# Kernel tuning notes

Measured on AMD Instinct MI355X. Metric: run time of the kernel, lower is better.

Reference implementation:

```python
import jax, jax.numpy as jnp
import numpy as np

_EPSILON = 1e-06


def _allocation(usage):
    """Freeness-based allocation: sort usage, exclusive cumprod, scatter back.

    usage: [B, M] in [0, 1]. Returns allocation weights [B, M].
    """
    usage = _EPSILON + (1.0 - _EPSILON) * usage
    nonusage = 1.0 - usage
    m = usage.shape[-1]
    sorted_nonusage, indices = jax.lax.top_k(nonusage, k=m)  # descending nonusage = ascending usage
    sorted_usage = 1.0 - sorted_nonusage
    # exclusive cumulative product along the sorted memory axis
    prod_sorted_usage = jnp.concatenate(
        [jnp.ones_like(sorted_usage[:, :1]),
         jnp.cumprod(sorted_usage, axis=1)[:, :-1]], axis=1)
    sorted_allocation = sorted_nonusage * prod_sorted_usage
    # invert the permutation and gather back to original slot order
    inverse_indices = jnp.argsort(indices, axis=1)
    return jnp.take_along_axis(sorted_allocation, inverse_indices, axis=1)


def _updated_usage(write_weights, free_gate, read_weights, prev_usage):
    """Freeness.__call__: usage after write then after read/free. [B, M]."""
    ww = jax.lax.stop_gradient(write_weights)
    # usage after write: increase toward 1 at written slots
    write_w = 1.0 - jnp.prod(1.0 - ww, axis=1)          # [B, M]
    usage = prev_usage + (1.0 - prev_usage) * write_w
    # usage after read: decrease where free_gate*read_weights is high
    free_read = free_gate[:, :, None] * read_weights      # [B, R, M]
    phi = jnp.prod(1.0 - free_read, axis=1)               # [B, M]
    return usage * phi


def _write_allocation_weights(usage, write_gates, num_writes):
    """Per-write-head allocation weights. Returns [B, num_writes, M]."""
    wg = write_gates[:, :, None]                          # [B, W, 1]
    allocs = []
    for i in range(num_writes):  # small fixed head count; sequential by construction
        a = _allocation(usage)
        allocs.append(a)
        usage = usage + (1.0 - usage) * wg[:, i, :] * a
    return jnp.stack(allocs, axis=1)


def setup_inputs() -> dict:
    key = jax.random.key(0)
    ks = jax.random.split(key, 5)
    B, W, R, M = 512, 4, 8, 16384
    return {
        "write_weights": jax.random.uniform(ks[0], (B, W, M), dtype=jnp.float32),
        "free_gate": jax.random.uniform(ks[1], (B, R), dtype=jnp.float32),
        "read_weights": jax.random.uniform(ks[2], (B, R, M), dtype=jnp.float32),
        "prev_usage": jax.random.uniform(ks[3], (B, M), dtype=jnp.float32),
        "write_gates": jax.random.uniform(ks[4], (B, W), dtype=jnp.float32),
        "num_writes": W,
    }


def reference(write_weights, free_gate, read_weights, prev_usage, write_gates, num_writes):
    usage = _updated_usage(write_weights, free_gate, read_weights, prev_usage)
    alloc = _write_allocation_weights(usage, write_gates, num_writes)
    return usage, alloc
```

## Files before the change

### kernel.cpp

```cpp
#include <hip/hip_runtime.h>
#include <stdint.h>

typedef unsigned long long u64;
typedef unsigned int u32;

#define NBINS 512
#define CAP 512
#define LOG_CUT (-64.0f)
#define LOG_SCALE 20.0f
#define NT 512

template <int TW, int TR>
__global__ __launch_bounds__(NT, 4)
void fused_kernel(const float* __restrict__ ww,
                  const float* __restrict__ fg,
                  const float* __restrict__ rw,
                  const float* __restrict__ prev,
                  const float* __restrict__ wgt,
                  float* __restrict__ out_usage,
                  float* __restrict__ out_alloc,
                  int B, int W, int R, int M)
{
    __shared__ u64   keyS[CAP];
    __shared__ float logS[CAP];
    __shared__ u32   hC[NBINS];
    __shared__ u32   tc[8];
    __shared__ float tw[8];
    __shared__ int   misc[4];
    extern __shared__ float uS[];

    const int Wl = TW > 0 ? TW : W;
    const int Rl = TR > 0 ? TR : R;
    const int b = blockIdx.x;
    const int t = threadIdx.x;
    const int lane = t & 63;
    const int wid = t >> 6;

    const float C1 = (float)(1.0 - 1e-6);
    const float CE = 1e-6f;

    {
        const size_t rowOff = (size_t)b * M;
        float frs[TR > 0 ? TR : 8];
        if (TR > 0)
            #pragma unroll
            for (int r = 0; r < Rl; ++r) frs[r] = fg[(size_t)b * Rl + r];

        const float4 z = make_float4(0.f, 0.f, 0.f, 0.f);
        for (int m = t * 4; m < M; m += NT * 4) {
            const float4 pv = *(const float4*)(prev + rowOff + m);
            float pr0 = 1.f, pr1 = 1.f, pr2 = 1.f, pr3 = 1.f;
            #pragma unroll
            for (int w = 0; w < Wl; ++w) {
                const float4 a = *(const float4*)(ww + ((size_t)b * Wl + w) * M + m);
                pr0 *= (1.0f - a.x); pr1 *= (1.0f - a.y);
                pr2 *= (1.0f - a.z); pr3 *= (1.0f - a.w);
            }
            float u0 = pv.x + (1.0f - pv.x) * (1.0f - pr0);
            float u1 = pv.y + (1.0f - pv.y) * (1.0f - pr1);
            float u2 = pv.z + (1.0f - pv.z) * (1.0f - pr2);
            float u3 = pv.w + (1.0f - pv.w) * (1.0f - pr3);
            float f0 = 1.f, f1 = 1.f, f2 = 1.f, f3 = 1.f;
            #pragma unroll
            for (int r = 0; r < Rl; ++r) {
                const float fr = (TR > 0) ? frs[r] : fg[(size_t)b * Rl + r];
                const float4 a = *(const float4*)(rw + ((size_t)b * Rl + r) * M + m);
                f0 *= (1.0f - fr * a.x); f1 *= (1.0f - fr * a.y);
                f2 *= (1.0f - fr * a.z); f3 *= (1.0f - fr * a.w);
            }
            float4 uo;
            uo.x = u0 * f0; uo.y = u1 * f1; uo.z = u2 * f2; uo.w = u3 * f3;
            *(float4*)(uS + m) = uo;
            *(float4*)(out_usage + rowOff + m) = uo;
            #pragma unroll
            for (int w = 0; w < Wl; ++w)
                *(float4*)(out_alloc + ((size_t)b * Wl + w) * M + m) = z;
        }
    }

    for (int i = 0; i < Wl; ++i) {
        const float wgi = wgt[(size_t)b * Wl + i];
        float* orow = out_alloc + ((size_t)b * Wl + i) * M;

        hC[t] = 0u;
        if (t == 0) { misc[0] = 0; misc[1] = -1; misc[2] = NBINS; }
        __syncthreads();

        for (int x = t * 4; x < M; x += NT * 4) {
            const float4 uu = *(const float4*)(uS + x);
            const float ua[4] = {uu.x, uu.y, uu.z, uu.w};
            #pragma unroll
            for (int j = 0; j < 4; ++j) {
                const float ue = CE + C1 * ua[j];
                const float lg = __log2f(ue);
                int bkt = (int)(-lg * LOG_SCALE);
                bkt = bkt < 0 ? 0 : (bkt > NBINS - 1 ? NBINS - 1 : bkt);
                atomicAdd(&hC[bkt], 1u);
            }
        }
        __syncthreads();

        {
            const int x = NBINS - 1 - t;
            const u32 c = hC[x];
            u32 sc = c;
            float sw = -(float)x * (1.0f / LOG_SCALE) * (float)c;
            #pragma unroll
            for (int off = 1; off < 64; off <<= 1) {
                const u32  oc = __shfl_up(sc, off);
                const float ow = __shfl_up(sw, off);
                if (lane >= off) { sc += oc; sw += ow; }
            }
            if (lane == 63) { tc[wid] = sc; tw[wid] = sw; }
            __syncthreads();
            u32 ac = 0; float aw = 0.f;
            for (int q = 0; q < wid; ++q) { ac += tc[q]; aw += tw[q]; }
            sc += ac; sw += aw;
            if (sw <= LOG_CUT) atomicMax(&misc[1], x);
            if (sc <= (u32)CAP) atomicMin(&misc[2], x);
        }
        __syncthreads();
        const int xs = misc[1];
        const int xc = misc[2];
        const int cut = (xs > xc) ? xs : xc;

        for (int x = t; x < M; x += NT) {
            const float u = uS[x];
            const float ue = CE + C1 * u;
            const float lg = __log2f(ue);
            int bkt = (int)(-lg * LOG_SCALE);
            bkt = bkt < 0 ? 0 : (bkt > NBINS - 1 ? NBINS - 1 : bkt);
            const bool pred = (bkt >= cut) && (cut < NBINS);
            const u64 mask = __ballot(pred);
            const int cnt = __popcll(mask);
            if (cnt) {
                int base = 0;
                if (lane == 0) base = atomicAdd(&misc[0], cnt);
                base = __shfl(base, 0);
                if (pred) {
                    const int pos = base + __popcll(mask & ((1ull << lane) - 1));
                    if (pos < CAP) {
                        const float nn = 1.0f - ue;
                        keyS[pos] = (((u64)(~__float_as_uint(nn))) << 14) | (u64)(u32)x;
                        logS[pos] = lg;
                    }
                }
            }
        }
        __syncthreads();
        int K = misc[0]; if (K > CAP) K = CAP;

        if (t < K) {
            const u64 mykey = keyS[t];
            float S = 0.0f;
            #pragma unroll 4
            for (int k = 0; k < K; ++k) {
                const u64 kk = keyS[k];
                const float lg = logS[k];
                if (kk < mykey) S += lg;
            }
            const float nn = __uint_as_float(~((u32)(mykey >> 14)));
            const int idx = (int)(mykey & 0x3FFFull);
            const float al = nn * __builtin_exp2f(S);
            if (al != 0.0f) {
                orow[idx] = al;
                const float u0v = uS[idx];
                uS[idx] = u0v + ((1.0f - u0v) * wgi) * al;
            }
        }
        __syncthreads();
    }
}

extern "C" void kernel_launch(void* const* d_in, const int* in_sizes, int n_in,
                              void* d_out, int out_size, void* d_ws, size_t ws_size,
                              hipStream_t stream) {
    const float* ww   = (const float*)d_in[0];
    const float* fg   = (const float*)d_in[1];
    const float* rw   = (const float*)d_in[2];
    const float* prev = (const float*)d_in[3];
    const float* wgt  = (const float*)d_in[4];
    const int BWM = in_sizes[0];
    const int BR  = in_sizes[1];
    const int BM  = in_sizes[3];
    const int BW  = in_sizes[4];
    const int M = BWM / BW;
    const int B = BM / M;
    const int W = BW / B;
    const int R = BR / B;

    float* out_usage = (float*)d_out;
    float* out_alloc = out_usage + (size_t)BM;

    const size_t smem = (size_t)M * sizeof(float);
    if (W == 4 && R == 8) {
        hipLaunchKernelGGL((fused_kernel<4, 8>), dim3(B), dim3(NT), smem, stream,
                           ww, fg, rw, prev, wgt, out_usage, out_alloc, B, W, R, M);
    } else {
        hipLaunchKernelGGL((fused_kernel<0, 0>), dim3(B), dim3(NT), smem, stream,
                           ww, fg, rw, prev, wgt, out_usage, out_alloc, B, W, R, M);
    }
}
```

Measured before the change: 163.2 us.

## Write allocation rows densely from shared bitmap instead of zero-fill plus scatter

Drops the upfront zero-fill of all allocation rows and the scattered global stores of the sparse nonzero entries. A per-row bitmap of selected slots plus a prefix-sum rank places each candidate value in compact shared storage, and a final pass writes each full row with float4 stores. Inputs for the usage phase are now loaded all at once before computing, which allows more loads in flight. In exchange it adds extra shared-memory passes, a shared atomicOr per candidate, and additional synchronisation per write head.

After: 168.5 us. +3.3%, slower.

```diff
diff --git a/kernel.cpp b/kernel.cpp
--- a/kernel.cpp
+++ b/kernel.cpp
@@ -9,6 +9,8 @@
 #define LOG_CUT (-64.0f)
 #define LOG_SCALE 20.0f
 #define NT 512
+#define NWAVE (NT / 64)
+#define MAXW 256
 
 template <int TW, int TR>
 __global__ __launch_bounds__(NT, 4)
@@ -23,9 +25,12 @@
 {
     __shared__ u64   keyS[CAP];
     __shared__ float logS[CAP];
+    __shared__ float valS[CAP];
     __shared__ u32   hC[NBINS];
-    __shared__ u32   tc[8];
-    __shared__ float tw[8];
+    __shared__ u64   bmS[MAXW];
+    __shared__ u32   boS[MAXW];
+    __shared__ u32   tc[NWAVE];
+    __shared__ float twv[NWAVE];
     __shared__ int   misc[4];
     extern __shared__ float uS[];
 
@@ -35,26 +40,35 @@
     const int t = threadIdx.x;
     const int lane = t & 63;
     const int wid = t >> 6;
+    const int MW = M >> 6;
 
     const float C1 = (float)(1.0 - 1e-6);
     const float CE = 1e-6f;
 
     {
         const size_t rowOff = (size_t)b * M;
+        const float* wp0 = ww + (size_t)b * Wl * M;
+        const float* rp0 = rw + (size_t)b * Rl * M;
         float frs[TR > 0 ? TR : 8];
-        if (TR > 0)
-            #pragma unroll
-            for (int r = 0; r < Rl; ++r) frs[r] = fg[(size_t)b * Rl + r];
-
-        const float4 z = make_float4(0.f, 0.f, 0.f, 0.f);
+        #pragma unroll
+        for (int r = 0; r < Rl; ++r) frs[r] = fg[(size_t)b * Rl + r];
+
         for (int m = t * 4; m < M; m += NT * 4) {
             const float4 pv = *(const float4*)(prev + rowOff + m);
+            float4 wv[TW > 0 ? TW : 4];
+            float4 rv[TR > 0 ? TR : 8];
+            #pragma unroll
+            for (int w = 0; w < Wl; ++w)
+                wv[w] = *(const float4*)(wp0 + (size_t)w * M + m);
+            #pragma unroll
+            for (int r = 0; r < Rl; ++r)
+                rv[r] = *(const float4*)(rp0 + (size_t)r * M + m);
+
             float pr0 = 1.f, pr1 = 1.f, pr2 = 1.f, pr3 = 1.f;
             #pragma unroll
             for (int w = 0; w < Wl; ++w) {
-                const float4 a = *(const float4*)(ww + ((size_t)b * Wl + w) * M + m);
-                pr0 *= (1.0f - a.x); pr1 *= (1.0f - a.y);
-                pr2 *= (1.0f - a.z); pr3 *= (1.0f - a.w);
+                pr0 *= (1.0f - wv[w].x); pr1 *= (1.0f - wv[w].y);
+                pr2 *= (1.0f - wv[w].z); pr3 *= (1.0f - wv[w].w);
             }
             float u0 = pv.x + (1.0f - pv.x) * (1.0f - pr0);
             float u1 = pv.y + (1.0f - pv.y) * (1.0f - pr1);
@@ -63,18 +77,14 @@
             float f0 = 1.f, f1 = 1.f, f2 = 1.f, f3 = 1.f;
             #pragma unroll
             for (int r = 0; r < Rl; ++r) {
-                const float fr = (TR > 0) ? frs[r] : fg[(size_t)b * Rl + r];
-                const float4 a = *(const float4*)(rw + ((size_t)b * Rl + r) * M + m);
-                f0 *= (1.0f - fr * a.x); f1 *= (1.0f - fr * a.y);
-                f2 *= (1.0f - fr * a.z); f3 *= (1.0f - fr * a.w);
+                const float fr = frs[r];
+                f0 *= (1.0f - fr * rv[r].x); f1 *= (1.0f - fr * rv[r].y);
+                f2 *= (1.0f - fr * rv[r].z); f3 *= (1.0f - fr * rv[r].w);
             }
             float4 uo;
             uo.x = u0 * f0; uo.y = u1 * f1; uo.z = u2 * f2; uo.w = u3 * f3;
             *(float4*)(uS + m) = uo;
             *(float4*)(out_usage + rowOff + m) = uo;
-            #pragma unroll
-            for (int w = 0; w < Wl; ++w)
-                *(float4*)(out_alloc + ((size_t)b * Wl + w) * M + m) = z;
         }
     }
 
@@ -83,6 +93,7 @@
         float* orow = out_alloc + ((size_t)b * Wl + i) * M;
 
         hC[t] = 0u;
+        for (int x = t; x < MW; x += NT) bmS[x] = 0ull;
         if (t == 0) { misc[0] = 0; misc[1] = -1; misc[2] = NBINS; }
         __syncthreads();
 
@@ -111,10 +122,10 @@
                 const float ow = __shfl_up(sw, off);
                 if (lane >= off) { sc += oc; sw += ow; }
             }
-            if (lane == 63) { tc[wid] = sc; tw[wid] = sw; }
+            if (lane == 63) { tc[wid] = sc; twv[wid] = sw; }
             __syncthreads();
             u32 ac = 0; float aw = 0.f;
-            for (int q = 0; q < wid; ++q) { ac += tc[q]; aw += tw[q]; }
+            for (int q = 0; q < wid; ++q) { ac += tc[q]; aw += twv[q]; }
             sc += ac; sw += aw;
             if (sw <= LOG_CUT) atomicMax(&misc[1], x);
             if (sc <= (u32)CAP) atomicMin(&misc[2], x);
@@ -143,12 +154,32 @@
                         const float nn = 1.0f - ue;
                         keyS[pos] = (((u64)(~__float_as_uint(nn))) << 14) | (u64)(u32)x;
                         logS[pos] = lg;
+                        atomicOr(&bmS[x >> 6], 1ull << (x & 63));
                     }
                 }
             }
         }
         __syncthreads();
         int K = misc[0]; if (K > CAP) K = CAP;
+
+        u32 myinc = 0, mycnt = 0;
+        if (t < MW) {
+            mycnt = (u32)__popcll(bmS[t]);
+            myinc = mycnt;
+            #pragma unroll
+            for (int off = 1; off < 64; off <<= 1) {
+                const u32 o = __shfl_up(myinc, off);
+                if (lane >= off) myinc += o;
+            }
+            if (lane == 63) tc[wid] = myinc;
+        }
+        __syncthreads();
+        if (t < MW) {
+            u32 add = 0;
+            for (int q = 0; q < wid; ++q) add += tc[q];
+            boS[t] = myinc + add - mycnt;
+        }
+        __syncthreads();
 
         if (t < K) {
             const u64 mykey = keyS[t];
@@ -162,11 +193,33 @@
             const float nn = __uint_as_float(~((u32)(mykey >> 14)));
             const int idx = (int)(mykey & 0x3FFFull);
             const float al = nn * __builtin_exp2f(S);
+            const u64 wbits = bmS[idx >> 6];
+            const int xr = (int)boS[idx >> 6]
+                         + (int)__popcll(wbits & ((1ull << (idx & 63)) - 1));
+            valS[xr] = al;
             if (al != 0.0f) {
-                orow[idx] = al;
                 const float u0v = uS[idx];
                 uS[idx] = u0v + ((1.0f - u0v) * wgi) * al;
             }
+        }
+        __syncthreads();
+
+        for (int x4 = t * 4; x4 < M; x4 += NT * 4) {
+            float4 o;
+            float* op = (float*)&o;
+            #pragma unroll
+            for (int j = 0; j < 4; ++j) {
+                const int x = x4 + j;
+                const u64 wbits = bmS[x >> 6];
+                float v = 0.0f;
+                if ((wbits >> (x & 63)) & 1ull) {
+                    const int xr = (int)boS[x >> 6]
+                                 + (int)__popcll(wbits & ((1ull << (x & 63)) - 1));
+                    v = valS[xr];
+                }
+                op[j] = v;
+            }
+            *(float4*)(orow + x4) = o;
         }
         __syncthreads();
     }
```
